# Performance work log

Measured on AMD Instinct MI355X. Metric: run time of the kernel, lower is better.

The kernel has to match this reference:

```python
import jax, jax.numpy as jnp
import numpy as np

N = 4096
INPUT_DIM = 512
KEY_DIM = 64
OUT_DIM = 512
N_HEADS = 8


def _xavier_normal(key, shape, gain):
    # torch xavier_normal_ on [heads, fan_in, fan_out]: fan over last two dims
    fan_in, fan_out = shape[-2], shape[-1]
    std = gain * (2.0 / (fan_in + fan_out)) ** 0.5
    return jax.random.normal(key, shape, dtype=jnp.float32) * std


def setup_inputs() -> dict:
    key = jax.random.key(0)
    kx, ka, kk, kq, kv, ko = jax.random.split(key, 6)
    gain = 2.0 ** 0.5
    node_matrix = jax.random.normal(kx, (N, INPUT_DIM), dtype=jnp.float32)
    adjacency_matrix = jax.random.randint(ka, (N, N), 0, 2).astype(jnp.float32)
    Wks = _xavier_normal(kk, (N_HEADS, INPUT_DIM, KEY_DIM), gain)
    Wqs = _xavier_normal(kq, (N_HEADS, INPUT_DIM, KEY_DIM), gain)
    Wvs = _xavier_normal(kv, (N_HEADS, INPUT_DIM, KEY_DIM), gain)
    Wo = _xavier_normal(ko, (N_HEADS, KEY_DIM, OUT_DIM), gain)
    return {"node_matrix": node_matrix, "adjacency_matrix": adjacency_matrix,
            "Wks": Wks, "Wqs": Wqs, "Wvs": Wvs, "Wo": Wo}


def reference(node_matrix, adjacency_matrix, Wks, Wqs, Wvs, Wo):
    n = adjacency_matrix.shape[0]
    # force self-loops
    adj = jnp.maximum(adjacency_matrix, jnp.eye(n, dtype=adjacency_matrix.dtype))
    # per-head projections: [heads, N, key_dim]
    keys = jnp.einsum('nj,hjk->hnk', node_matrix, Wks)
    queries = jnp.einsum('nj,hjk->hnk', node_matrix, Wqs)
    values = jnp.einsum('nj,hjk->hnk', node_matrix, Wvs)
    key_dim = Wks.shape[-1]
    # [heads, N(query), N(key)] scores, scaled and adjacency-masked
    atts = jnp.einsum('hqk,hmk->hqm', queries, keys) / (key_dim ** 0.5)
    atts = atts - 1e16 * (1.0 - adj)[None, :, :]
    atts = jax.nn.softmax(atts, axis=-1)
    # weighted values, then output projection, summed over heads -> [N, out_dim]
    return jnp.einsum('hqm,hmk,hko->qo', atts, values, Wo)
```

## Files before the change

### kernel.cpp

```cpp
#include <hip/hip_runtime.h>
#include <stdint.h>

typedef unsigned short u16;
typedef __attribute__((ext_vector_type(8))) __bf16 bf16x8;
typedef __attribute__((ext_vector_type(8))) short short8;
typedef __attribute__((ext_vector_type(4))) float f32x4;

#define N_NODES 4096
#define DMODEL  512
#define QKVLD   1536
#define KD      64
#define NH      8
#define NSPLIT  4
#define LOG2E   1.4426950408889634f

static __device__ __forceinline__ u16 f2bf(float f) {
  unsigned u = __builtin_bit_cast(unsigned, f);
  u += 0x7fffu + ((u >> 16) & 1u);
  return (u16)(u >> 16);
}

static __device__ __forceinline__ f32x4 mfma16(short8 a, short8 b, f32x4 c) {
  return __builtin_amdgcn_mfma_f32_16x16x32_bf16(
      __builtin_bit_cast(bf16x8, a), __builtin_bit_cast(bf16x8, b), c, 0, 0, 0);
}

static __device__ __forceinline__ void gload16(const u16* g, u16* l) {
  __builtin_amdgcn_global_load_lds((const __attribute__((address_space(1))) void*)g,
                                   (__attribute__((address_space(3))) void*)l, 16, 0, 0);
}

static __device__ __forceinline__ short8 cvt8(float4 a, float4 b) {
  unsigned p0, p1, p2, p3;
  asm("v_cvt_pk_bf16_f32 %0, %1, %2" : "=v"(p0) : "v"(a.x), "v"(a.y));
  asm("v_cvt_pk_bf16_f32 %0, %1, %2" : "=v"(p1) : "v"(a.z), "v"(a.w));
  asm("v_cvt_pk_bf16_f32 %0, %1, %2" : "=v"(p2) : "v"(b.x), "v"(b.y));
  asm("v_cvt_pk_bf16_f32 %0, %1, %2" : "=v"(p3) : "v"(b.z), "v"(b.w));
  uint4 u; u.x = p0; u.y = p1; u.z = p2; u.w = p3;
  return __builtin_bit_cast(short8, u);
}

__global__ void pack_w(const float* __restrict__ Wq, const float* __restrict__ Wk,
                       const float* __restrict__ Wv, const float* __restrict__ Wo,
                       u16* __restrict__ Wt, u16* __restrict__ Wot) {
  __shared__ float t[64][65];
  int z = blockIdx.z;
  int tid = threadIdx.x, lc = tid & 63;
  if (z < 24) {
    int mat = z >> 3, h = z & 7;
    const float* src = (mat == 0) ? Wq : ((mat == 1) ? Wk : Wv);
    float scale = (mat == 0) ? 0.125f * LOG2E : 1.0f;
    src += (size_t)h * DMODEL * KD;
    u16* dst = Wt + ((size_t)mat * DMODEL + (size_t)h * KD) * DMODEL;
    int r0 = blockIdx.x * 64;
#pragma unroll
    for (int i = 0; i < 16; ++i) {
      int row = i * 4 + (tid >> 6);
      t[row][lc] = src[(size_t)(r0 + row) * KD + lc];
    }
    __syncthreads();
#pragma unroll
    for (int i = 0; i < 16; ++i) {
      int row = i * 4 + (tid >> 6);
      dst[(size_t)row * DMODEL + r0 + lc] = f2bf(t[lc][row] * scale);
    }
  } else {
    int r0 = (z - 24) * 64, c0 = blockIdx.x * 64;
#pragma unroll
    for (int i = 0; i < 16; ++i) {
      int row = i * 4 + (tid >> 6);
      t[row][lc] = Wo[(size_t)(r0 + row) * 512 + c0 + lc];
    }
    __syncthreads();
#pragma unroll
    for (int i = 0; i < 16; ++i) {
      int row = i * 4 + (tid >> 6);
      Wot[(size_t)(c0 + row) * 512 + r0 + lc] = f2bf(t[lc][row]);
    }
  }
}

__global__ void build_bits(const float* __restrict__ adj, unsigned long long* __restrict__ bits) {
  int gw = (blockIdx.x * blockDim.x + threadIdx.x) >> 6;
  int lane = threadIdx.x & 63;
  int nw = (gridDim.x * blockDim.x) >> 6;
  for (int word = gw; word < N_NODES * 64; word += nw) {
    int q = word >> 6, wc = word & 63;
    int k = wc * 64 + lane;
    float v = adj[(size_t)q * N_NODES + k];
    unsigned long long m = __ballot((v != 0.0f) || (q == k));
    if (lane == 0) bits[word] = m;
  }
}

__global__ __launch_bounds__(256) void gemm_qkv(const float* __restrict__ X,
                                                const u16* __restrict__ Bt,
                                                u16* __restrict__ C,
                                                u16* __restrict__ Vt) {
  __shared__ __align__(16) u16 lA[64 * 64];
  __shared__ __align__(16) u16 lB[64 * 64];
  const int m0 = blockIdx.x * 64, n0 = blockIdx.y * 64;
  const int tid = threadIdx.x;
  const int w = tid >> 6, lane = tid & 63, lm = lane & 15, lg = lane >> 4;
  const int srow = tid >> 2, sc0 = tid & 3;
  f32x4 acc[4] = {};
  for (int k0 = 0; k0 < 512; k0 += 64) {
    __syncthreads();
    {
      const float4* ga = (const float4*)(X + (size_t)(m0 + srow) * 512 + k0);
      short8 s1 = cvt8(ga[2 * sc0], ga[2 * sc0 + 1]);
      short8 s2 = cvt8(ga[2 * (sc0 + 4)], ga[2 * (sc0 + 4) + 1]);
      short8* la = (short8*)(lA + srow * 64);
      la[sc0 ^ (srow & 7)] = s1;
      la[(sc0 + 4) ^ (srow & 7)] = s2;
      const short8* gb = (const short8*)(Bt + (size_t)(n0 + srow) * 512 + k0);
      short8* lb = (short8*)(lB + srow * 64);
      lb[sc0 ^ (srow & 7)] = gb[sc0];
      lb[(sc0 + 4) ^ (srow & 7)] = gb[sc0 + 4];
    }
    __syncthreads();
    short8 af0, af1;
    {
      int row = w * 16 + lm;
      af0 = ((short8*)(lA + row * 64))[lg ^ (row & 7)];
      af1 = ((short8*)(lA + row * 64))[(4 + lg) ^ (row & 7)];
    }
#pragma unroll
    for (int nt = 0; nt < 4; ++nt) {
      int row = nt * 16 + lm;
      short8 b0 = ((short8*)(lB + row * 64))[lg ^ (row & 7)];
      short8 b1 = ((short8*)(lB + row * 64))[(4 + lg) ^ (row & 7)];
      acc[nt] = mfma16(af0, b0, acc[nt]);
      acc[nt] = mfma16(af1, b1, acc[nt]);
    }
  }
#pragma unroll
  for (int nt = 0; nt < 4; ++nt) {
    int n = n0 + nt * 16 + lm;
    int mb = m0 + w * 16 + lg * 4;
    ushort4 o4;
#pragma unroll
    for (int r = 0; r < 4; ++r) ((u16*)&o4)[r] = f2bf(acc[nt][r]);
#pragma unroll
    for (int r = 0; r < 4; ++r) C[(size_t)(mb + r) * QKVLD + n] = ((u16*)&o4)[r];
    if (n >= 1024)
      *(ushort4*)(Vt + (size_t)(n - 1024) * N_NODES + mb) = o4;
  }
}

__global__ __launch_bounds__(256) void gemm_out(const u16* __restrict__ A,
                                                const u16* __restrict__ Bt,
                                                float* __restrict__ C) {
  __shared__ __align__(16) u16 lA[64 * 64];
  __shared__ __align__(16) u16 lB[64 * 64];
  const int m0 = blockIdx.x * 64, n0 = blockIdx.y * 64;
  const int tid = threadIdx.x;
  const int w = tid >> 6, lane = tid & 63, lm = lane & 15, lg = lane >> 4;
  const int srow = tid >> 2, sc0 = tid & 3;
  f32x4 acc[4] = {};
  for (int k0 = 0; k0 < 512; k0 += 64) {
    __syncthreads();
    {
      const short8* ga = (const short8*)(A + (size_t)(m0 + srow) * 512 + k0);
      short8* la = (short8*)(lA + srow * 64);
      la[sc0 ^ (srow & 7)] = ga[sc0];
      la[(sc0 + 4) ^ (srow & 7)] = ga[sc0 + 4];
      const short8* gb = (const short8*)(Bt + (size_t)(n0 + srow) * 512 + k0);
      short8* lb = (short8*)(lB + srow * 64);
      lb[sc0 ^ (srow & 7)] = gb[sc0];
      lb[(sc0 + 4) ^ (srow & 7)] = gb[sc0 + 4];
    }
    __syncthreads();
    short8 af0, af1;
    {
      int row = w * 16 + lm;
      af0 = ((short8*)(lA + row * 64))[lg ^ (row & 7)];
      af1 = ((short8*)(lA + row * 64))[(4 + lg) ^ (row & 7)];
    }
#pragma unroll
    for (int nt = 0; nt < 4; ++nt) {
      int row = nt * 16 + lm;
      short8 b0 = ((short8*)(lB + row * 64))[lg ^ (row & 7)];
      short8 b1 = ((short8*)(lB + row * 64))[(4 + lg) ^ (row & 7)];
      acc[nt] = mfma16(af0, b0, acc[nt]);
      acc[nt] = mfma16(af1, b1, acc[nt]);
    }
  }
#pragma unroll
  for (int nt = 0; nt < 4; ++nt) {
    int n = n0 + nt * 16 + lm;
    int mb = m0 + w * 16 + lg * 4;
#pragma unroll
    for (int r = 0; r < 4; ++r)
      C[(size_t)(mb + r) * 512 + n] = acc[nt][r];
  }
}

__global__ __launch_bounds__(512, 4) void attn_kernel(const u16* __restrict__ QKV,
                                                      const u16* __restrict__ Vt,
                                                      const unsigned long long* __restrict__ bits,
                                                      float* __restrict__ Op,
                                                      float* __restrict__ lp) {
  __shared__ __align__(16) u16 LDSA[16384 + 8 * 2304];
  const int bid = blockIdx.x;
  const int h = bid & 7, sp = (bid >> 3) & 3, qb = bid >> 5;
  const int tid = threadIdx.x;
  const int w = tid >> 6, lane = tid & 63, lm = lane & 15, lg = lane >> 4;
  const int lg4 = lg * 4;
  const int kb0 = sp * 16;

  const int q0 = qb * 256 + w * 32 + lm;
  const int q1 = q0 + 16;

  const short8 qf00 = *(const short8*)(QKV + (size_t)q0 * QKVLD + h * 64 + lg * 8);
  const short8 qf01 = *(const short8*)(QKV + (size_t)q0 * QKVLD + h * 64 + 32 + lg * 8);
  const short8 qf10 = *(const short8*)(QKV + (size_t)q1 * QKVLD + h * 64 + lg * 8);
  const short8 qf11 = *(const short8*)(QKV + (size_t)q1 * QKVLD + h * 64 + 32 + lg * 8);

  short8 ones;
#pragma unroll
  for (int j = 0; j < 8; ++j) ones[j] = (short)0x3F80;

  const int a0 = lm * 64 + (lg ^ (lm & 7)) * 8;
  const u16* rdA = LDSA + a0;
  const u16* rdB = LDSA + (a0 ^ 32);
  u16* pW0 = LDSA + 16384 + w * 2304 + lm * 72 + lg4;
  u16* pW1 = pW0 + 1152;
  const u16* pR0 = LDSA + 16384 + w * 2304 + lm * 72 + lg * 8;
  const u16* pR1 = pR0 + 1152;

  const int srow = lane >> 3, sc = lane & 7;
  const int grow = w * 8 + srow;
  const u16* kP = QKV + (size_t)(kb0 * 64 + grow) * QKVLD + 512 + h * 64 + (sc ^ srow) * 8;
  const u16* vP = Vt + ((size_t)h * 64 + grow) * N_NODES + kb0 * 64 + (sc ^ srow) * 8;

#define STAGE(buf) do {                                   \
    gload16(kP, LDSA + (buf) * 4096 + w * 512);           \
    gload16(vP, LDSA + 8192 + (buf) * 4096 + w * 512);    \
  } while (0)
#define ADV() do { kP += 64 * QKVLD; vP += 64; } while (0)

  f32x4 of0[4] = {}, of1[4] = {};
  f32x4 la0 = {}, la1 = {};
  const unsigned long long* bp0 = bits + (size_t)q0 * 64 + kb0;
  const unsigned long long* bp1 = bits + (size_t)q1 * 64 + kb0;

  STAGE(0);
  unsigned long long wb0 = bp0[0], wb1 = bp1[0];

#define SMPACK(sv, wbv, pW, pR, la, paA, paB)                                  \
  do {                                                                         \
    unsigned wlo = (unsigned)((wbv) >> lg4);                                   \
    unsigned whi = ((unsigned)((wbv) >> 32)) >> lg4;                           \
    _Pragma("unroll")                                                          \
    for (int kt = 0; kt < 4; ++kt) {                                           \
      unsigned word = (kt < 2) ? wlo : whi;                                    \
      float pv[4];                                                             \
      _Pragma("unroll")                                                        \
      for (int r = 0; r < 4; ++r) {                                            \
        float e = __builtin_amdgcn_exp2f(sv[kt][r]);                           \
        int mb;                                                                \
        asm("v_bfe_i32 %0, %1, %2, 1" : "=v"(mb)                               \
            : "v"(word), "n"((kt & 1) * 16 + r));                              \
        pv[r] = __builtin_bit_cast(float,                                      \
                   __builtin_bit_cast(unsigned, e) & (unsigned)mb);            \
      }                                                                        \
      unsigned pk0, pk1;                                                       \
      asm("v_cvt_pk_bf16_f32 %0, %1, %2" : "=v"(pk0) : "v"(pv[0]), "v"(pv[1]));\
      asm("v_cvt_pk_bf16_f32 %0, %1, %2" : "=v"(pk1) : "v"(pv[2]), "v"(pv[3]));\
      uint2 pr; pr.x = pk0; pr.y = pk1;                                        \
      *(uint2*)(pW + kt * 16) = pr;                                            \
    }                                                                          \
    paA = *(const short8*)(pR);                                                \
    paB = *(const short8*)(pR + 32);                                           \
    la = mfma16(ones, paA, la);                                                \
    la = mfma16(ones, paB, la);                                                \
  } while (0)

#define BODY(buf, i)                                                           \
  do {                                                                         \
    asm volatile("s_waitcnt vmcnt(0)" ::: "memory");                           \
    __builtin_amdgcn_s_barrier();                                              \
    if ((i) + 1 < 16) { ADV(); STAGE(buf ^ 1); }                               \
    unsigned long long nb0 = ((i) + 1 < 16) ? bp0[(i) + 1] : 0ull;             \
    unsigned long long nb1 = ((i) + 1 < 16) ? bp1[(i) + 1] : 0ull;             \
    f32x4 s0[4], s1[4];                                                        \
    _Pragma("unroll")                                                          \
    for (int kt = 0; kt < 4; ++kt) {                                           \
      short8 k0 = *(const short8*)(rdA + (buf) * 4096 + kt * 1024);            \
      short8 k1 = *(const short8*)(rdB + (buf) * 4096 + kt * 1024);            \
      f32x4 z0 = {0.f, 0.f, 0.f, 0.f}, z1 = {0.f, 0.f, 0.f, 0.f};              \
      z0 = mfma16(k0, qf00, z0); s0[kt] = mfma16(k1, qf01, z0);                \
      z1 = mfma16(k0, qf10, z1); s1[kt] = mfma16(k1, qf11, z1);                \
    }                                                                          \
    short8 pa00, pa01, pa10, pa11;                                             \
    SMPACK(s0, wb0, pW0, pR0, la0, pa00, pa01);                                \
    SMPACK(s1, wb1, pW1, pR1, la1, pa10, pa11);                                \
    _Pragma("unroll")                                                          \
    for (int dt = 0; dt < 4; ++dt) {                                           \
      short8 v0 = *(const short8*)(rdA + 8192 + (buf) * 4096 + dt * 1024);     \
      short8 v1 = *(const short8*)(rdB + 8192 + (buf) * 4096 + dt * 1024);     \
      of0[dt] = mfma16(v0, pa00, of0[dt]);                                     \
      of0[dt] = mfma16(v1, pa01, of0[dt]);                                     \
      of1[dt] = mfma16(v0, pa10, of1[dt]);                                     \
      of1[dt] = mfma16(v1, pa11, of1[dt]);                                     \
    }                                                                          \
    wb0 = nb0; wb1 = nb1;                                                      \
  } while (0)

#pragma unroll 1
  for (int it = 0; it < 8; ++it) {
    BODY(0, it * 2);
    BODY(1, it * 2 + 1);
  }
#undef BODY
#undef SMPACK
#undef STAGE
#undef ADV

  float* Ob = Op + (size_t)sp * N_NODES * DMODEL;
#pragma unroll
  for (int dt = 0; dt < 4; ++dt) {
    *(f32x4*)(Ob + (size_t)q0 * DMODEL + h * 64 + dt * 16 + lg4) = of0[dt];
    *(f32x4*)(Ob + (size_t)q1 * DMODEL + h * 64 + dt * 16 + lg4) = of1[dt];
  }
  if (lg == 0) {
    lp[((size_t)sp * NH + h) * N_NODES + q0] = la0[0];
    lp[((size_t)sp * NH + h) * N_NODES + q1] = la1[0];
  }
}

__global__ __launch_bounds__(256) void combine_kernel(const float* __restrict__ Op,
                                                      const float* __restrict__ lp,
                                                      u16* __restrict__ Oc) {
  int i = blockIdx.x * 256 + threadIdx.x;
  int col = (i * 4) & (DMODEL - 1);
  int q = (i * 4) >> 9;
  int h = col >> 6;
  float4 acc = {0.f, 0.f, 0.f, 0.f};
  float l = 0.f;
#pragma unroll
  for (int sp = 0; sp < NSPLIT; ++sp) {
    float4 a = ((const float4*)(Op + (size_t)sp * N_NODES * DMODEL))[i];
    acc.x += a.x; acc.y += a.y; acc.z += a.z; acc.w += a.w;
    l += lp[((size_t)sp * NH + h) * N_NODES + q];
  }
  float inv = 1.0f / l;
  ushort4 o;
  o.x = f2bf(acc.x * inv);
  o.y = f2bf(acc.y * inv);
  o.z = f2bf(acc.z * inv);
  o.w = f2bf(acc.w * inv);
  ((ushort4*)Oc)[i] = o;
}


extern "C" void kernel_launch(void* const* d_in, const int* in_sizes, int n_in,
                              void* d_out, int out_size, void* d_ws, size_t ws_size,
                              hipStream_t stream) {
  const float* X   = (const float*)d_in[0];
  const float* Adj = (const float*)d_in[1];
  const float* Wks = (const float*)d_in[2];
  const float* Wqs = (const float*)d_in[3];
  const float* Wvs = (const float*)d_in[4];
  const float* Wo  = (const float*)d_in[5];

  char* p = (char*)d_ws;
  u16* Wt  = (u16*)p; p += (size_t)3 * DMODEL * DMODEL * 2;
  u16* Wot = (u16*)p; p += (size_t)DMODEL * DMODEL * 2;
  u16* QKV = (u16*)p; p += (size_t)N_NODES * QKVLD * 2;
  u16* Vt  = (u16*)p; p += (size_t)N_NODES * DMODEL * 2;
  u16* Oc  = (u16*)p; p += (size_t)N_NODES * DMODEL * 2;
  unsigned long long* bits = (unsigned long long*)p; p += (size_t)N_NODES * 64 * 8;
  float* Op = (float*)p; p += (size_t)NSPLIT * N_NODES * DMODEL * 4;
  float* lp = (float*)p; p += (size_t)NSPLIT * NH * N_NODES * 4;

  pack_w<<<dim3(8, 1, 32), dim3(256), 0, stream>>>(Wqs, Wks, Wvs, Wo, Wt, Wot);
  build_bits<<<dim3(2048), dim3(256), 0, stream>>>(Adj, bits);

  gemm_qkv<<<dim3(64, 24), dim3(256), 0, stream>>>(X, Wt, QKV, Vt);

  attn_kernel<<<dim3(512), dim3(512), 0, stream>>>(QKV, Vt, bits, Op, lp);
  combine_kernel<<<dim3(N_NODES * DMODEL / 4 / 256), dim3(256), 0, stream>>>(Op, lp, Oc);

  gemm_out<<<dim3(64, 8), dim3(256), 0, stream>>>(Oc, Wot, (float*)d_out);
}
```

Baseline: 109.5 us.

## Enlarge QKV GEMM tile to 128x128 with direct-to-LDS B loads

The QKV projection GEMM moves from 64x64 tiles to 128x128 tiles, with each wave computing a 64x64 sub-tile of 4x4 MFMA fragments. This raises register-level reuse and cuts redundant global reads of X and weights. The B operand is now loaded with a gload16 direct-to-LDS helper, pre-swizzled and followed by an explicit vmcnt wait. The grid shrinks to 384 blocks, which may leave some CUs idle, and the larger accumulator set raises register pressure.

Measured after the change: 114.9 us. 1.05x slower.

```diff
diff --git a/kernel.cpp b/kernel.cpp
--- a/kernel.cpp
+++ b/kernel.cpp
@@ -97,55 +97,73 @@
                                                 const u16* __restrict__ Bt,
                                                 u16* __restrict__ C,
                                                 u16* __restrict__ Vt) {
-  __shared__ __align__(16) u16 lA[64 * 64];
-  __shared__ __align__(16) u16 lB[64 * 64];
-  const int m0 = blockIdx.x * 64, n0 = blockIdx.y * 64;
+  __shared__ __align__(16) u16 lA[128 * 64];
+  __shared__ __align__(16) u16 lB[128 * 64];
+  const int m0 = blockIdx.x * 128, n0 = blockIdx.y * 128;
   const int tid = threadIdx.x;
   const int w = tid >> 6, lane = tid & 63, lm = lane & 15, lg = lane >> 4;
-  const int srow = tid >> 2, sc0 = tid & 3;
-  f32x4 acc[4] = {};
+  const int wr = w >> 1, wc = w & 1;
+  const int arow = tid >> 1, ac0 = (tid & 1) * 4;
+  const int brow = lane >> 3;
+  const int bchunk = (lane & 7) ^ brow;
+  const u16* bSrc[4];
+#pragma unroll
+  for (int i = 0; i < 4; ++i)
+    bSrc[i] = Bt + (size_t)(n0 + w * 32 + i * 8 + brow) * 512 + bchunk * 8;
+  const int a0 = lm * 64 + (lg ^ (lm & 7)) * 8;
+  const u16* raA = lA + wr * 4096 + a0;
+  const u16* raB = lA + wr * 4096 + (a0 ^ 32);
+  const u16* rbA = lB + wc * 4096 + a0;
+  const u16* rbB = lB + wc * 4096 + (a0 ^ 32);
+
+  f32x4 acc[4][4] = {};
   for (int k0 = 0; k0 < 512; k0 += 64) {
     __syncthreads();
     {
-      const float4* ga = (const float4*)(X + (size_t)(m0 + srow) * 512 + k0);
-      short8 s1 = cvt8(ga[2 * sc0], ga[2 * sc0 + 1]);
-      short8 s2 = cvt8(ga[2 * (sc0 + 4)], ga[2 * (sc0 + 4) + 1]);
-      short8* la = (short8*)(lA + srow * 64);
-      la[sc0 ^ (srow & 7)] = s1;
-      la[(sc0 + 4) ^ (srow & 7)] = s2;
-      const short8* gb = (const short8*)(Bt + (size_t)(n0 + srow) * 512 + k0);
-      short8* lb = (short8*)(lB + srow * 64);
-      lb[sc0 ^ (srow & 7)] = gb[sc0];
-      lb[(sc0 + 4) ^ (srow & 7)] = gb[sc0 + 4];
-    }
-    __syncthreads();
-    short8 af0, af1;
-    {
-      int row = w * 16 + lm;
-      af0 = ((short8*)(lA + row * 64))[lg ^ (row & 7)];
-      af1 = ((short8*)(lA + row * 64))[(4 + lg) ^ (row & 7)];
-    }
-#pragma unroll
-    for (int nt = 0; nt < 4; ++nt) {
-      int row = nt * 16 + lm;
-      short8 b0 = ((short8*)(lB + row * 64))[lg ^ (row & 7)];
-      short8 b1 = ((short8*)(lB + row * 64))[(4 + lg) ^ (row & 7)];
-      acc[nt] = mfma16(af0, b0, acc[nt]);
-      acc[nt] = mfma16(af1, b1, acc[nt]);
-    }
-  }
-#pragma unroll
-  for (int nt = 0; nt < 4; ++nt) {
-    int n = n0 + nt * 16 + lm;
-    int mb = m0 + w * 16 + lg * 4;
-    ushort4 o4;
-#pragma unroll
-    for (int r = 0; r < 4; ++r) ((u16*)&o4)[r] = f2bf(acc[nt][r]);
-#pragma unroll
-    for (int r = 0; r < 4; ++r) C[(size_t)(mb + r) * QKVLD + n] = ((u16*)&o4)[r];
-    if (n >= 1024)
-      *(ushort4*)(Vt + (size_t)(n - 1024) * N_NODES + mb) = o4;
-  }
+      const float4* ga = (const float4*)(X + (size_t)(m0 + arow) * 512 + k0);
+      short8* la = (short8*)(lA + arow * 64);
+#pragma unroll
+      for (int j = 0; j < 4; ++j) {
+        int c = ac0 + j;
+        la[c ^ (arow & 7)] = cvt8(ga[2 * c], ga[2 * c + 1]);
+      }
+#pragma unroll
+      for (int i = 0; i < 4; ++i)
+        gload16(bSrc[i] + k0, lB + (w * 32 + i * 8) * 64);
+    }
+    asm volatile("s_waitcnt vmcnt(0)" ::: "memory");
+    __syncthreads();
+    short8 af[4][2], bf[4][2];
+#pragma unroll
+    for (int f = 0; f < 4; ++f) {
+      af[f][0] = *(const short8*)(raA + f * 1024);
+      af[f][1] = *(const short8*)(raB + f * 1024);
+      bf[f][0] = *(const short8*)(rbA + f * 1024);
+      bf[f][1] = *(const short8*)(rbB + f * 1024);
+    }
+#pragma unroll
+    for (int fr = 0; fr < 4; ++fr)
+#pragma unroll
+      for (int fc = 0; fc < 4; ++fc) {
+        acc[fr][fc] = mfma16(af[fr][0], bf[fc][0], acc[fr][fc]);
+        acc[fr][fc] = mfma16(af[fr][1], bf[fc][1], acc[fr][fc]);
+      }
+  }
+  const bool isV = (n0 >= 1024);
+#pragma unroll
+  for (int fr = 0; fr < 4; ++fr)
+#pragma unroll
+    for (int fc = 0; fc < 4; ++fc) {
+      int n = n0 + wc * 64 + fc * 16 + lm;
+      int mb = m0 + wr * 64 + fr * 16 + lg * 4;
+      ushort4 o4;
+#pragma unroll
+      for (int r = 0; r < 4; ++r) ((u16*)&o4)[r] = f2bf(acc[fr][fc][r]);
+#pragma unroll
+      for (int r = 0; r < 4; ++r) C[(size_t)(mb + r) * QKVLD + n] = ((u16*)&o4)[r];
+      if (isV)
+        *(ushort4*)(Vt + (size_t)(n - 1024) * N_NODES + mb) = o4;
+    }
 }
 
 __global__ __launch_bounds__(256) void gemm_out(const u16* __restrict__ A,
@@ -378,7 +396,7 @@
   pack_w<<<dim3(8, 1, 32), dim3(256), 0, stream>>>(Wqs, Wks, Wvs, Wo, Wt, Wot);
   build_bits<<<dim3(2048), dim3(256), 0, stream>>>(Adj, bits);
 
-  gemm_qkv<<<dim3(64, 24), dim3(256), 0, stream>>>(X, Wt, QKV, Vt);
+  gemm_qkv<<<dim3(32, 12), dim3(256), 0, stream>>>(X, Wt, QKV, Vt);
 
   attn_kernel<<<dim3(512), dim3(512), 0, stream>>>(QKV, Vt, bits, Op, lp);
   combine_kernel<<<dim3(N_NODES * DMODEL / 4 / 256), dim3(256), 0, stream>>>(Op, lp, Oc);
```
